# Kernel optimization log

Hardware: AMD Instinct MI355X
Metric: run time of the kernel (lower is better)

Reference implementation:

```python
import jax, jax.numpy as jnp
import numpy as np

N_NODES = 50000
N_EDGES = 640000
D_IN = 128
D_H1 = 128
D_H2 = 256
NEG_SLOPE = 0.2


def setup_inputs() -> dict:
    key = jax.random.key(0)
    ks = jax.random.split(key, 12)
    s = 1.0 / np.sqrt(D_IN)
    inp = {
        'x': jax.random.normal(ks[0], (N_NODES, D_IN), dtype=jnp.float32),
        'edge_index': jax.random.randint(ks[1], (2, N_EDGES), 0, N_NODES, dtype=jnp.int64),
        # GATv2 layer 1: 128 -> 128 (separate lin_l / lin_r, attention vec, residual proj, bias)
        'Wl1': jax.random.normal(ks[2], (D_IN, D_H1), dtype=jnp.float32) * s,
        'Wr1': jax.random.normal(ks[3], (D_IN, D_H1), dtype=jnp.float32) * s,
        'att1': jax.random.normal(ks[4], (D_H1,), dtype=jnp.float32) * s,
        'Wres1': jax.random.normal(ks[5], (D_IN, D_H1), dtype=jnp.float32) * s,
        'b1': jnp.zeros((D_H1,), dtype=jnp.float32),
        # GATv2 layer 2: 128 -> 256
        'Wl2': jax.random.normal(ks[6], (D_H1, D_H2), dtype=jnp.float32) * s,
        'Wr2': jax.random.normal(ks[7], (D_H1, D_H2), dtype=jnp.float32) * s,
        'att2': jax.random.normal(ks[8], (D_H2,), dtype=jnp.float32) * s,
        'Wres2': jax.random.normal(ks[9], (D_H1, D_H2), dtype=jnp.float32) * s,
        'b2': jnp.zeros((D_H2,), dtype=jnp.float32),
    }
    return inp


def _gatv2_layer(x, Wl, Wr, att, Wres, b, src, dst, n_nodes):
    """GATv2Conv (heads=1, residual=True, eval mode/no dropout).
    score e_ij = att . LeakyReLU(Wl x_src + Wr x_dst); softmax over incoming edges per dst;
    out_dst = sum_j alpha_ij * (Wl x_src) + residual + bias.
    """
    xl = x @ Wl                      # [N, F]
    xr = x @ Wr                      # [N, F]
    h = xl[src] + xr[dst]            # [E, F]  gather (irregular access)
    e = jax.nn.leaky_relu(h, NEG_SLOPE) @ att   # [E]
    # segment softmax over destination nodes
    m = jax.ops.segment_max(e, dst, num_segments=n_nodes)      # [N]
    w = jnp.exp(e - m[dst])                                     # [E]
    denom = jax.ops.segment_sum(w, dst, num_segments=n_nodes)   # [N]
    alpha = w / (denom[dst] + 1e-16)                             # [E]
    out = jax.ops.segment_sum(alpha[:, None] * xl[src], dst, num_segments=n_nodes)  # [N, F]
    return out + x @ Wres + b


def reference(x, edge_index, Wl1, Wr1, att1, Wres1, b1, Wl2, Wr2, att2, Wres2, b2):
    src = edge_index[0]
    dst = edge_index[1]
    h = _gatv2_layer(x, Wl1, Wr1, att1, Wres1, b1, src, dst, N_NODES)
    h = jax.nn.elu(h)
    out = _gatv2_layer(h, Wl2, Wr2, att2, Wres2, b2, src, dst, N_NODES)
    return out
```

## Files before the change

### kernel.cpp

```cpp
#include <hip/hip_runtime.h>

typedef unsigned short u16;
typedef unsigned int u32;
typedef __attribute__((ext_vector_type(8))) short bf16x8;
typedef __attribute__((ext_vector_type(4))) float f32x4;
typedef __attribute__((ext_vector_type(2))) float f32x2;

#define NN 50000
#define NE 640000

__device__ __forceinline__ float bfl(u32 u) { return __uint_as_float(u << 16); }
__device__ __forceinline__ float bfh(u32 u) { return __uint_as_float(u & 0xffff0000u); }
__device__ __forceinline__ float bf1(u16 v) { return __uint_as_float(((u32)v) << 16); }
__device__ __forceinline__ u16 f2bf(float f) {
  u32 u = __float_as_uint(f);
  u32 r = (u + 0x7fffu + ((u >> 16) & 1u)) >> 16;
  return (u16)r;
}

__device__ __forceinline__ f32x2 bc2(float s) { return (f32x2){s, s}; }
__device__ __forceinline__ f32x2 pkfma(f32x2 a, f32x2 b, f32x2 c) {
  return __builtin_elementwise_fma(a, b, c);
}
__device__ __forceinline__ f32x2 pkabs(f32x2 a) {
  return __builtin_elementwise_abs(a);
}

template <int CTRL>
__device__ __forceinline__ float dpp_add(float x) {
  int t = __builtin_amdgcn_update_dpp(0, __float_as_int(x), CTRL, 0xf, 0xf, true);
  return x + __int_as_float(t);
}

__device__ __forceinline__ void unpk2(uint2 v, f32x2* o) {
  o[0] = (f32x2){bfl(v.x), bfh(v.x)};
  o[1] = (f32x2){bfl(v.y), bfh(v.y)};
}
__device__ __forceinline__ void unpk2(uint4 v, f32x2* o) {
  o[0] = (f32x2){bfl(v.x), bfh(v.x)};
  o[1] = (f32x2){bfl(v.y), bfh(v.y)};
  o[2] = (f32x2){bfl(v.z), bfh(v.z)};
  o[3] = (f32x2){bfl(v.w), bfh(v.w)};
}

template <int HEPL> struct VecSel;
template <> struct VecSel<4> { using T = uint2; };
template <> struct VecSel<8> { using T = uint4; };

__global__ void probe_kernel(const u16* __restrict__ x, const int* __restrict__ ei,
                             int* __restrict__ flags) {
  __shared__ int s_f32, s_i32;
  if (threadIdx.x == 0) { s_f32 = 0; s_i32 = 0; }
  __syncthreads();
  int lf = 0, li = 0;
  for (int i = threadIdx.x; i < 1024; i += 256) {
    float v = bf1(x[i]);
    if (!(fabsf(v) < 1e8f)) lf = 1;
    if (ei[2 * i + 1] != 0) li = 1;
  }
  if (lf) s_f32 = 1;
  if (li) s_i32 = 1;
  __syncthreads();
  if (threadIdx.x == 0) {
    flags[0] = s_f32;
    flags[1] = s_i32 ? 0 : 1;
  }
}

__device__ __forceinline__ int edge_val(const int* __restrict__ w, long j, int i64) {
  return i64 ? w[2 * j] : w[j];
}

__global__ void count_kernel(const int* __restrict__ ei, const int* __restrict__ flags,
                             int* __restrict__ cnt, int E) {
  int e = blockIdx.x * blockDim.x + threadIdx.x;
  if (e >= E) return;
  int d = edge_val(ei, (long)E + e, flags[1]);
  if ((u32)d < (u32)NN) atomicAdd(&cnt[d], 1);
}

__global__ void scan_local(const int* __restrict__ cnt, int* __restrict__ excl,
                           int* __restrict__ bsum, int n) {
  __shared__ int sd[256];
  int t = threadIdx.x;
  int g = blockIdx.x * 256 + t;
  int v = (g < n) ? cnt[g] : 0;
  sd[t] = v;
  __syncthreads();
  for (int off = 1; off < 256; off <<= 1) {
    int x = (t >= off) ? sd[t - off] : 0;
    __syncthreads();
    sd[t] += x;
    __syncthreads();
  }
  int incl = sd[t];
  if (g < n) excl[g] = incl - v;
  if (t == 255) bsum[blockIdx.x] = incl;
}

__global__ void scan_totals(const int* __restrict__ bsum, int* __restrict__ boff, int nb) {
  __shared__ int sd[256];
  int t = threadIdx.x;
  int v = (t < nb) ? bsum[t] : 0;
  sd[t] = v;
  __syncthreads();
  for (int off = 1; off < 256; off <<= 1) {
    int x = (t >= off) ? sd[t - off] : 0;
    __syncthreads();
    sd[t] += x;
    __syncthreads();
  }
  if (t < nb) boff[t] = sd[t] - v;
}

__global__ void scan_add(const int* __restrict__ excl, const int* __restrict__ boff,
                         const int* __restrict__ cnt, int* __restrict__ rowptr,
                         int* __restrict__ fillp, int n) {
  int g = blockIdx.x * 256 + threadIdx.x;
  if (g < n) {
    int e2 = excl[g] + boff[blockIdx.x];
    rowptr[g] = e2;
    fillp[g] = e2;
    if (g == n - 1) rowptr[n] = e2 + cnt[g];
  }
}

__global__ void fill_kernel(const int* __restrict__ ei, const int* __restrict__ flags,
                            int* __restrict__ fillp, int* __restrict__ col, int E) {
  int e = blockIdx.x * blockDim.x + threadIdx.x;
  if (e >= E) return;
  int i64 = flags[1];
  int s = edge_val(ei, (long)e, i64);
  int d = edge_val(ei, (long)E + e, i64);
  if ((u32)d >= (u32)NN) return;
  int p = atomicAdd(&fillp[d], 1);
  col[p] = ((u32)s < (u32)NN) ? s : 0;
}

__global__ void transpose_w(const void* W0, const void* W1, const void* W2,
                            const void* W3, const void* W4, const void* W5,
                            u16* T0, u16* T1, u16* T2, u16* T3, u16* T4, u16* T5,
                            const int* __restrict__ flags) {
  int y = blockIdx.y;
  int M = (y < 3) ? 128 : 256;
  int flat = blockIdx.x * 256 + threadIdx.x;
  if (flat >= M * 128) return;
  int j = flat >> 7;
  int k = flat & 127;
  const void* W = (y == 0) ? W0 : (y == 1) ? W1 : (y == 2) ? W2 : (y == 3) ? W3 : (y == 4) ? W4 : W5;
  u16* T = (y == 0) ? T0 : (y == 1) ? T1 : (y == 2) ? T2 : (y == 3) ? T3 : (y == 4) ? T4 : T5;
  u16 v;
  if (flags[0])
    v = f2bf(((const float*)W)[(size_t)k * M + j]);
  else
    v = ((const u16*)W)[(size_t)k * M + j];
  T[(size_t)j * 128 + k] = v;
}

#define LSTR 136
__global__ __launch_bounds__(256) void gemm3_mfma(
    const void* __restrict__ X,
    const u16* __restrict__ Wta, const u16* __restrict__ Wtb, const u16* __restrict__ Wtc,
    const void* __restrict__ bias,
    u16* __restrict__ Ya, u16* __restrict__ Yb, u16* __restrict__ Yc,
    const int* __restrict__ flags, int x_follows, int N, int M) {
  __shared__ __align__(16) u16 Xs[64 * LSTR];
  __shared__ __align__(16) u16 Bs[128 * LSTR];
  const int K = 128;
  int t = threadIdx.x;
  int lane = t & 63;
  int w = t >> 6;
  int n0g = blockIdx.x * 64;
  int c0 = blockIdx.z * 128;
  int F32X = x_follows ? flags[0] : 0;
  const u16* Wt = (blockIdx.y == 0) ? Wta : ((blockIdx.y == 1) ? Wtb : Wtc);
  u16* Y = (blockIdx.y == 0) ? Ya : ((blockIdx.y == 1) ? Yb : Yc);

  if (!F32X) {
    const u16* Xg = (const u16*)X;
    for (int it = 0; it < 4; ++it) {
      int i = t + 256 * it;
      int r = i >> 4, c8 = (i & 15) * 8;
      int n = n0g + r;
      uint4 v = make_uint4(0, 0, 0, 0);
      if (n < N) v = *(const uint4*)(Xg + (size_t)n * K + c8);
      *(uint4*)(Xs + r * LSTR + c8) = v;
    }
  } else {
    const float* Xg = (const float*)X;
    for (int it = 0; it < 4; ++it) {
      int i = t + 256 * it;
      int r = i >> 4, c8 = (i & 15) * 8;
      int n = n0g + r;
      uint4 pk = make_uint4(0, 0, 0, 0);
      if (n < N) {
        float4 f0 = *(const float4*)(Xg + (size_t)n * K + c8);
        float4 f1 = *(const float4*)(Xg + (size_t)n * K + c8 + 4);
        pk.x = (u32)f2bf(f0.x) | ((u32)f2bf(f0.y) << 16);
        pk.y = (u32)f2bf(f0.z) | ((u32)f2bf(f0.w) << 16);
        pk.z = (u32)f2bf(f1.x) | ((u32)f2bf(f1.y) << 16);
        pk.w = (u32)f2bf(f1.z) | ((u32)f2bf(f1.w) << 16);
      }
      *(uint4*)(Xs + r * LSTR + c8) = pk;
    }
  }
  for (int it = 0; it < 8; ++it) {
    int i = t + 256 * it;
    int j = i >> 4, k8 = (i & 15) * 8;
    uint4 v = *(const uint4*)(Wt + (size_t)(c0 + j) * K + k8);
    *(uint4*)(Bs + j * LSTR + k8) = v;
  }
  __syncthreads();

  int m0 = (w >> 1) * 32;
  int n0 = (w & 1) * 64;
  int l15 = lane & 15;
  int q8 = (lane >> 4) * 8;
  f32x4 acc[2][4];
#pragma unroll
  for (int i = 0; i < 2; ++i)
#pragma unroll
    for (int j = 0; j < 4; ++j) acc[i][j] = (f32x4){0.f, 0.f, 0.f, 0.f};

#pragma unroll
  for (int kc = 0; kc < 4; ++kc) {
    int ko = kc * 32 + q8;
    bf16x8 a[2], b[4];
#pragma unroll
    for (int i = 0; i < 2; ++i)
      a[i] = *(const bf16x8*)(Xs + (m0 + i * 16 + l15) * LSTR + ko);
#pragma unroll
    for (int j = 0; j < 4; ++j)
      b[j] = *(const bf16x8*)(Bs + (n0 + j * 16 + l15) * LSTR + ko);
#pragma unroll
    for (int i = 0; i < 2; ++i)
#pragma unroll
      for (int j = 0; j < 4; ++j)
        acc[i][j] = __builtin_amdgcn_mfma_f32_16x16x32_bf16(a[i], b[j], acc[i][j], 0, 0, 0);
  }
  __syncthreads();

  float bv[4] = {0.f, 0.f, 0.f, 0.f};
  if (blockIdx.y == 2) {
    int F32 = flags[0];
#pragma unroll
    for (int j = 0; j < 4; ++j) {
      int c = c0 + n0 + j * 16 + l15;
      bv[j] = F32 ? ((const float*)bias)[c] : bf1(((const u16*)bias)[c]);
    }
  }

  u16* Ct = Xs;
#pragma unroll
  for (int i = 0; i < 2; ++i)
#pragma unroll
    for (int j = 0; j < 4; ++j) {
      int col = n0 + j * 16 + l15;
      int rbase = m0 + i * 16 + (lane >> 4) * 4;
#pragma unroll
      for (int r = 0; r < 4; ++r)
        Ct[(rbase + r) * LSTR + col] = f2bf(acc[i][j][r] + bv[j]);
    }
  __syncthreads();

  for (int it = 0; it < 4; ++it) {
    int i = t + 256 * it;
    int r = i >> 4, c8 = (i & 15) * 8;
    int n = n0g + r;
    if (n < N) {
      uint4 v = *(const uint4*)(Ct + r * LSTR + c8);
      *(uint4*)(Y + (size_t)n * M + c0 + c8) = v;
    }
  }
}

template <int F, bool ELU>
__global__ __launch_bounds__(256) void gat_agg_kernel(
    const u16* __restrict__ xl, const u16* __restrict__ xr, const u16* __restrict__ res,
    const void* __restrict__ att, const int* __restrict__ rowptr, const int* __restrict__ col,
    void* __restrict__ out, const int* __restrict__ flags, int out_follows, int N) {
  constexpr int HEPL = F / 32;
  constexpr int HP = HEPL / 2;
  using VecT = typename VecSel<HEPL>::T;
  int tid = threadIdx.x;
  int hl = tid & 31;
  int node = blockIdx.x * 8 + (tid >> 5);
  if (node >= N) return;
  int F32 = flags[0];
  int OF32 = out_follows ? F32 : 0;
  int base = hl * HEPL;

  f32x2 xr2[HP], att6[HP], att4[HP], acc2[HP];
  {
    VecT xp = *(const VecT*)(xr + (size_t)node * F + base);
    unpk2(xp, xr2);
  }
  if (F32) {
    const float* af = (const float*)att + base;
#pragma unroll
    for (int p = 0; p < HP; ++p) {
      f32x2 a = (f32x2){af[2 * p], af[2 * p + 1]};
      att6[p] = a * 0.6f;
      att4[p] = a * 0.4f;
    }
  } else {
    f32x2 a2[HP];
    VecT ap = *(const VecT*)((const u16*)att + base);
    unpk2(ap, a2);
#pragma unroll
    for (int p = 0; p < HP; ++p) {
      att6[p] = a2[p] * 0.6f;
      att4[p] = a2[p] * 0.4f;
    }
  }
#pragma unroll
  for (int p = 0; p < HP; ++p) acc2[p] = bc2(0.f);

  float m = -1e30f, l = 0.f;
  int beg = rowptr[node], end = rowptr[node + 1];
  int deg = end - beg;

  if (deg > 0) {
    int nit = (deg + 1) >> 1;
    int dm1 = deg - 1;
    auto ldc = [&](int j) -> int { return col[beg + min(j, dm1)]; };
    auto gat = [&](int c) -> VecT { return *(const VecT*)(xl + (size_t)c * F + base); };

    int c0 = ldc(0), c1 = ldc(1), c2 = ldc(2), c3 = ldc(3);
    int c4 = ldc(4), c5 = ldc(5);
    VecT va = gat(c0), vb = gat(c1), vc = gat(c2), vd = gat(c3);

    for (int t = 0; t < nit; ++t) {
      VecT x0v = va, x1v = vb;
      int act1 = (2 * t + 1) < deg;
      va = vc; vb = vd;
      if (t + 2 < nit) { vc = gat(c4); vd = gat(c5); }
      if (t + 3 < nit) { c4 = ldc(2 * t + 6); c5 = ldc(2 * t + 7); }

      f32x2 x0[HP], x1[HP];
      unpk2(x0v, x0);
      unpk2(x1v, x1);
      f32x2 s0 = bc2(0.f), s1 = bc2(0.f);
#pragma unroll
      for (int p = 0; p < HP; ++p) {
        f32x2 h0 = x0[p] + xr2[p];
        f32x2 h1 = x1[p] + xr2[p];
        f32x2 ha0 = pkabs(h0);
        f32x2 ha1 = pkabs(h1);
        s0 = pkfma(att6[p], h0, s0);
        s1 = pkfma(att6[p], h1, s1);
        s0 = pkfma(att4[p], ha0, s0);
        s1 = pkfma(att4[p], ha1, s1);
      }
      float d0 = s0.x + s0.y;
      float d1 = s1.x + s1.y;
      d0 = dpp_add<0xB1>(d0);  d1 = dpp_add<0xB1>(d1);
      d0 = dpp_add<0x4E>(d0);  d1 = dpp_add<0x4E>(d1);
      d0 = dpp_add<0x141>(d0); d1 = dpp_add<0x141>(d1);
      d0 = dpp_add<0x140>(d0); d1 = dpp_add<0x140>(d1);
      d0 += __shfl_xor(d0, 16, 64);
      d1 += __shfl_xor(d1, 16, 64);

      float p0 = d0;
      float p1 = act1 ? d1 : -1e30f;
      float mn = fmaxf(m, fmaxf(p0, p1));
      float scl = __expf(m - mn);
      float w0 = __expf(p0 - mn);
      float w1 = __expf(p1 - mn);
      l = fmaf(l, scl, w0 + w1);
      f32x2 w0b = bc2(w0), w1b = bc2(w1), sclb = bc2(scl);
#pragma unroll
      for (int p = 0; p < HP; ++p)
        acc2[p] = pkfma(sclb, acc2[p], pkfma(w1b, x1[p], w0b * x0[p]));
      m = mn;
    }
  }

  float inv = 1.f / (l + 1e-16f);
  VecT rp = *(const VecT*)(res + (size_t)node * F + base);
  f32x2 rv[HP];
  unpk2(rp, rv);
  f32x2 ov[HP];
  f32x2 invb = bc2(inv);
#pragma unroll
  for (int p = 0; p < HP; ++p) {
    f32x2 o = pkfma(acc2[p], invb, rv[p]);
    if (ELU) {
      o.x = (o.x > 0.f) ? o.x : (__expf(o.x) - 1.f);
      o.y = (o.y > 0.f) ? o.y : (__expf(o.y) - 1.f);
    }
    ov[p] = o;
  }
  if (OF32) {
    float* of = (float*)out + (size_t)node * F + base;
    float4 f0 = {ov[0].x, ov[0].y, ov[1].x, ov[1].y};
    *(float4*)of = f0;
    if constexpr (HP == 4) {
      float4 f1 = {ov[2].x, ov[2].y, ov[3].x, ov[3].y};
      *(float4*)(of + 4) = f1;
    }
  } else {
    u16* o16 = (u16*)out;
    if constexpr (HP == 2) {
      uint2 pk;
      pk.x = (u32)f2bf(ov[0].x) | ((u32)f2bf(ov[0].y) << 16);
      pk.y = (u32)f2bf(ov[1].x) | ((u32)f2bf(ov[1].y) << 16);
      *(uint2*)(o16 + (size_t)node * F + base) = pk;
    } else {
      uint4 pk;
      pk.x = (u32)f2bf(ov[0].x) | ((u32)f2bf(ov[0].y) << 16);
      pk.y = (u32)f2bf(ov[1].x) | ((u32)f2bf(ov[1].y) << 16);
      pk.z = (u32)f2bf(ov[2].x) | ((u32)f2bf(ov[2].y) << 16);
      pk.w = (u32)f2bf(ov[3].x) | ((u32)f2bf(ov[3].y) << 16);
      *(uint4*)(o16 + (size_t)node * F + base) = pk;
    }
  }
}

extern "C" void kernel_launch(void* const* d_in, const int* in_sizes, int n_in,
                              void* d_out, int out_size, void* d_ws, size_t ws_size,
                              hipStream_t stream) {
  const u16* x16 = (const u16*)d_in[0];
  const int* ei = (const int*)d_in[1];
  const int N = NN, E = NE;

  char* ws = (char*)d_ws;
  size_t off = 0;
  auto alloc = [&](size_t bytes) -> void* {
    void* p = (void*)(ws + off);
    off += (bytes + 255) & ~(size_t)255;
    return p;
  };
  int* flags = (int*)alloc(2 * 4);
  int* cnt = (int*)alloc((size_t)N * 4);
  int* rowptr = (int*)alloc((size_t)(N + 1) * 4);
  int* fillp = (int*)alloc((size_t)N * 4);
  int* colb = (int*)alloc((size_t)E * 4);
  int* excl = (int*)alloc((size_t)N * 4);
  int* bsum = (int*)alloc(256 * 4);
  int* boff = (int*)alloc(256 * 4);
  u16* Wt1a = (u16*)alloc((size_t)128 * 128 * 2);
  u16* Wt1b = (u16*)alloc((size_t)128 * 128 * 2);
  u16* Wt1c = (u16*)alloc((size_t)128 * 128 * 2);
  u16* Wt2a = (u16*)alloc((size_t)256 * 128 * 2);
  u16* Wt2b = (u16*)alloc((size_t)256 * 128 * 2);
  u16* Wt2c = (u16*)alloc((size_t)256 * 128 * 2);
  u16* buf1 = (u16*)alloc((size_t)N * 256 * 2);
  u16* buf2 = (u16*)alloc((size_t)N * 256 * 2);
  u16* buf3 = (u16*)alloc((size_t)N * 256 * 2);
  u16* h1 = (u16*)alloc((size_t)N * 128 * 2);
  (void)ws_size; (void)n_in; (void)in_sizes; (void)out_size;

  int nb = (N + 255) / 256;

  probe_kernel<<<1, 256, 0, stream>>>(x16, ei, flags);
  hipMemsetAsync(cnt, 0, (size_t)N * 4, stream);
  count_kernel<<<(E + 255) / 256, 256, 0, stream>>>(ei, flags, cnt, E);
  scan_local<<<nb, 256, 0, stream>>>(cnt, excl, bsum, N);
  scan_totals<<<1, 256, 0, stream>>>(bsum, boff, nb);
  scan_add<<<nb, 256, 0, stream>>>(excl, boff, cnt, rowptr, fillp, N);
  fill_kernel<<<(E + 255) / 256, 256, 0, stream>>>(ei, flags, fillp, colb, E);
  transpose_w<<<dim3(128, 6), 256, 0, stream>>>(
      d_in[2], d_in[3], d_in[5], d_in[7], d_in[8], d_in[10],
      Wt1a, Wt1b, Wt1c, Wt2a, Wt2b, Wt2c, flags);

  int gx = (N + 63) / 64;
  gemm3_mfma<<<dim3(gx, 3, 1), 256, 0, stream>>>(
      d_in[0], Wt1a, Wt1b, Wt1c, d_in[6], buf1, buf2, buf3, flags, 1, N, 128);
  gat_agg_kernel<128, true><<<(N + 7) / 8, 256, 0, stream>>>(
      buf1, buf2, buf3, d_in[4], rowptr, colb, h1, flags, 0, N);
  gemm3_mfma<<<dim3(gx, 3, 2), 256, 0, stream>>>(
      h1, Wt2a, Wt2b, Wt2c, d_in[11], buf1, buf2, buf3, flags, 0, N, 256);
  gat_agg_kernel<256, false><<<(N + 7) / 8, 256, 0, stream>>>(
      buf1, buf2, buf3, d_in[9], rowptr, colb, d_out, flags, 1, N);
}
```

Measured before the change: 327.2 us.

## Fuse the three projection GEMMs per row tile to reuse staged X

Replaces the 3D grid, in which each block computed one weight and one column chunk, with a 512-thread block holding a 128-row X tile. That block loops over all three weight matrices and their column chunks, reusing the X tile from LDS. This removes the redundant reloads (and fp32-to-bf16 conversion) of X across the separate grid blocks. In exchange the grid is smaller, and each block runs the weight loads, MFMA and stores serially with several barriers per pass, so there is less parallelism and overlap.

```diff
diff --git a/kernel.cpp b/kernel.cpp
--- a/kernel.cpp
+++ b/kernel.cpp
@@ -158,28 +158,27 @@
 }
 
 #define LSTR 136
-__global__ __launch_bounds__(256) void gemm3_mfma(
+template <int MZ>
+__global__ __launch_bounds__(512) void gemm3_fused(
     const void* __restrict__ X,
     const u16* __restrict__ Wta, const u16* __restrict__ Wtb, const u16* __restrict__ Wtc,
     const void* __restrict__ bias,
     u16* __restrict__ Ya, u16* __restrict__ Yb, u16* __restrict__ Yc,
-    const int* __restrict__ flags, int x_follows, int N, int M) {
-  __shared__ __align__(16) u16 Xs[64 * LSTR];
+    const int* __restrict__ flags, int x_follows, int N) {
+  constexpr int M = MZ * 128;
+  __shared__ __align__(16) u16 Xs[128 * LSTR];
   __shared__ __align__(16) u16 Bs[128 * LSTR];
   const int K = 128;
   int t = threadIdx.x;
   int lane = t & 63;
   int w = t >> 6;
-  int n0g = blockIdx.x * 64;
-  int c0 = blockIdx.z * 128;
+  int n0g = blockIdx.x * 128;
   int F32X = x_follows ? flags[0] : 0;
-  const u16* Wt = (blockIdx.y == 0) ? Wta : ((blockIdx.y == 1) ? Wtb : Wtc);
-  u16* Y = (blockIdx.y == 0) ? Ya : ((blockIdx.y == 1) ? Yb : Yc);
 
   if (!F32X) {
     const u16* Xg = (const u16*)X;
     for (int it = 0; it < 4; ++it) {
-      int i = t + 256 * it;
+      int i = t + 512 * it;
       int r = i >> 4, c8 = (i & 15) * 8;
       int n = n0g + r;
       uint4 v = make_uint4(0, 0, 0, 0);
@@ -189,7 +188,7 @@
   } else {
     const float* Xg = (const float*)X;
     for (int it = 0; it < 4; ++it) {
-      int i = t + 256 * it;
+      int i = t + 512 * it;
       int r = i >> 4, c8 = (i & 15) * 8;
       int n = n0g + r;
       uint4 pk = make_uint4(0, 0, 0, 0);
@@ -204,72 +203,73 @@
       *(uint4*)(Xs + r * LSTR + c8) = pk;
     }
   }
-  for (int it = 0; it < 8; ++it) {
-    int i = t + 256 * it;
-    int j = i >> 4, k8 = (i & 15) * 8;
-    uint4 v = *(const uint4*)(Wt + (size_t)(c0 + j) * K + k8);
-    *(uint4*)(Bs + j * LSTR + k8) = v;
-  }
-  __syncthreads();
-
-  int m0 = (w >> 1) * 32;
-  int n0 = (w & 1) * 64;
+
   int l15 = lane & 15;
   int q8 = (lane >> 4) * 8;
-  f32x4 acc[2][4];
-#pragma unroll
-  for (int i = 0; i < 2; ++i)
-#pragma unroll
-    for (int j = 0; j < 4; ++j) acc[i][j] = (f32x4){0.f, 0.f, 0.f, 0.f};
-
-#pragma unroll
-  for (int kc = 0; kc < 4; ++kc) {
-    int ko = kc * 32 + q8;
-    bf16x8 a[2], b[4];
-#pragma unroll
-    for (int i = 0; i < 2; ++i)
-      a[i] = *(const bf16x8*)(Xs + (m0 + i * 16 + l15) * LSTR + ko);
-#pragma unroll
-    for (int j = 0; j < 4; ++j)
-      b[j] = *(const bf16x8*)(Bs + (n0 + j * 16 + l15) * LSTR + ko);
-#pragma unroll
-    for (int i = 0; i < 2; ++i)
-#pragma unroll
-      for (int j = 0; j < 4; ++j)
-        acc[i][j] = __builtin_amdgcn_mfma_f32_16x16x32_bf16(a[i], b[j], acc[i][j], 0, 0, 0);
-  }
-  __syncthreads();
-
-  float bv[4] = {0.f, 0.f, 0.f, 0.f};
-  if (blockIdx.y == 2) {
-    int F32 = flags[0];
-#pragma unroll
-    for (int j = 0; j < 4; ++j) {
-      int c = c0 + n0 + j * 16 + l15;
-      bv[j] = F32 ? ((const float*)bias)[c] : bf1(((const u16*)bias)[c]);
-    }
-  }
-
-  u16* Ct = Xs;
-#pragma unroll
-  for (int i = 0; i < 2; ++i)
-#pragma unroll
-    for (int j = 0; j < 4; ++j) {
-      int col = n0 + j * 16 + l15;
-      int rbase = m0 + i * 16 + (lane >> 4) * 4;
-#pragma unroll
-      for (int r = 0; r < 4; ++r)
-        Ct[(rbase + r) * LSTR + col] = f2bf(acc[i][j][r] + bv[j]);
-    }
-  __syncthreads();
-
-  for (int it = 0; it < 4; ++it) {
-    int i = t + 256 * it;
-    int r = i >> 4, c8 = (i & 15) * 8;
-    int n = n0g + r;
-    if (n < N) {
-      uint4 v = *(const uint4*)(Ct + r * LSTR + c8);
-      *(uint4*)(Y + (size_t)n * M + c0 + c8) = v;
+  int m0 = w * 16;
+  int F32B = flags[0];
+
+#pragma unroll
+  for (int z = 0; z < MZ; ++z) {
+#pragma unroll
+    for (int y = 0; y < 3; ++y) {
+      const u16* Wt = (y == 0) ? Wta : ((y == 1) ? Wtb : Wtc);
+      int c0 = z * 128;
+      for (int it = 0; it < 4; ++it) {
+        int i = t + 512 * it;
+        int j = i >> 4, k8 = (i & 15) * 8;
+        uint4 v = *(const uint4*)(Wt + (size_t)(c0 + j) * K + k8);
+        *(uint4*)(Bs + j * LSTR + k8) = v;
+      }
+      __syncthreads();
+
+      f32x4 acc[8];
+#pragma unroll
+      for (int j = 0; j < 8; ++j) acc[j] = (f32x4){0.f, 0.f, 0.f, 0.f};
+#pragma unroll
+      for (int kc = 0; kc < 4; ++kc) {
+        int ko = kc * 32 + q8;
+        bf16x8 a = *(const bf16x8*)(Xs + (m0 + l15) * LSTR + ko);
+        bf16x8 b[8];
+#pragma unroll
+        for (int j = 0; j < 8; ++j)
+          b[j] = *(const bf16x8*)(Bs + (j * 16 + l15) * LSTR + ko);
+#pragma unroll
+        for (int j = 0; j < 8; ++j)
+          acc[j] = __builtin_amdgcn_mfma_f32_16x16x32_bf16(a, b[j], acc[j], 0, 0, 0);
+      }
+      __syncthreads();
+
+      float bv[8] = {0.f, 0.f, 0.f, 0.f, 0.f, 0.f, 0.f, 0.f};
+      if (y == 2) {
+#pragma unroll
+        for (int j = 0; j < 8; ++j) {
+          int c = c0 + j * 16 + l15;
+          bv[j] = F32B ? ((const float*)bias)[c] : bf1(((const u16*)bias)[c]);
+        }
+      }
+      u16* Ct = Bs;
+      int rbase = m0 + (lane >> 4) * 4;
+#pragma unroll
+      for (int j = 0; j < 8; ++j) {
+        int colj = j * 16 + l15;
+#pragma unroll
+        for (int r = 0; r < 4; ++r)
+          Ct[(rbase + r) * LSTR + colj] = f2bf(acc[j][r] + bv[j]);
+      }
+      __syncthreads();
+
+      u16* Y = (y == 0) ? Ya : ((y == 1) ? Yb : Yc);
+      for (int it = 0; it < 4; ++it) {
+        int i = t + 512 * it;
+        int r = i >> 4, c8 = (i & 15) * 8;
+        int n = n0g + r;
+        if (n < N) {
+          uint4 v = *(const uint4*)(Ct + r * LSTR + c8);
+          *(uint4*)(Y + (size_t)n * M + c0 + c8) = v;
+        }
+      }
+      __syncthreads();
     }
   }
 }
@@ -464,13 +464,13 @@
       d_in[2], d_in[3], d_in[5], d_in[7], d_in[8], d_in[10],
       Wt1a, Wt1b, Wt1c, Wt2a, Wt2b, Wt2c, flags);
 
-  int gx = (N + 63) / 64;
-  gemm3_mfma<<<dim3(gx, 3, 1), 256, 0, stream>>>(
-      d_in[0], Wt1a, Wt1b, Wt1c, d_in[6], buf1, buf2, buf3, flags, 1, N, 128);
+  int gx = (N + 127) / 128;
+  gemm3_fused<1><<<gx, 512, 0, stream>>>(
+      d_in[0], Wt1a, Wt1b, Wt1c, d_in[6], buf1, buf2, buf3, flags, 1, N);
   gat_agg_kernel<128, true><<<(N + 7) / 8, 256, 0, stream>>>(
       buf1, buf2, buf3, d_in[4], rowptr, colb, h1, flags, 0, N);
-  gemm3_mfma<<<dim3(gx, 3, 2), 256, 0, stream>>>(
-      h1, Wt2a, Wt2b, Wt2c, d_in[11], buf1, buf2, buf3, flags, 0, N, 256);
+  gemm3_fused<2><<<gx, 512, 0, stream>>>(
+      h1, Wt2a, Wt2b, Wt2c, d_in[11], buf1, buf2, buf3, flags, 0, N);
   gat_agg_kernel<256, false><<<(N + 7) / 8, 256, 0, stream>>>(
       buf1, buf2, buf3, d_in[9], rowptr, colb, d_out, flags, 1, N);
 }
```

Measured after the change: 333.0 us. No clear change (+1.8%).

## Use 16-lane groups for layer-1 aggregation, fuse CSR scan, deepen gather prefetch

Applied to the files above, without the earlier changes.

Layer-1 aggregation now gives each node a 16-lane group with 16-byte loads per lane instead of 32 lanes with 8-byte loads. This halves the shuffle reductions per edge and doubles the nodes handled per block. The gather pipeline prefetches one more edge pair ahead to hide irregular load latency, at the cost of extra registers. The three-kernel scan that builds the CSR row pointers is replaced by a single 1024-thread block scan, cutting launches but serializing the work onto one workgroup.

```diff
diff --git a/kernel.cpp b/kernel.cpp
--- a/kernel.cpp
+++ b/kernel.cpp
@@ -32,20 +32,12 @@
   return x + __int_as_float(t);
 }
 
-__device__ __forceinline__ void unpk2(uint2 v, f32x2* o) {
-  o[0] = (f32x2){bfl(v.x), bfh(v.x)};
-  o[1] = (f32x2){bfl(v.y), bfh(v.y)};
-}
 __device__ __forceinline__ void unpk2(uint4 v, f32x2* o) {
   o[0] = (f32x2){bfl(v.x), bfh(v.x)};
   o[1] = (f32x2){bfl(v.y), bfh(v.y)};
   o[2] = (f32x2){bfl(v.z), bfh(v.z)};
   o[3] = (f32x2){bfl(v.w), bfh(v.w)};
 }
-
-template <int HEPL> struct VecSel;
-template <> struct VecSel<4> { using T = uint2; };
-template <> struct VecSel<8> { using T = uint4; };
 
 __global__ void probe_kernel(const u16* __restrict__ x, const int* __restrict__ ei,
                              int* __restrict__ flags) {
@@ -79,50 +71,31 @@
   if ((u32)d < (u32)NN) atomicAdd(&cnt[d], 1);
 }
 
-__global__ void scan_local(const int* __restrict__ cnt, int* __restrict__ excl,
-                           int* __restrict__ bsum, int n) {
-  __shared__ int sd[256];
+__global__ __launch_bounds__(1024) void scan_fused(const int* __restrict__ cnt,
+                                                   int* __restrict__ rowptr,
+                                                   int* __restrict__ fillp, int n) {
+  __shared__ int sums[1024];
   int t = threadIdx.x;
-  int g = blockIdx.x * 256 + t;
-  int v = (g < n) ? cnt[g] : 0;
-  sd[t] = v;
-  __syncthreads();
-  for (int off = 1; off < 256; off <<= 1) {
-    int x = (t >= off) ? sd[t - off] : 0;
+  int per = (n + 1023) / 1024;
+  int s0 = t * per;
+  int s1 = min(s0 + per, n);
+  int s = 0;
+  for (int i = s0; i < s1; ++i) s += cnt[i];
+  sums[t] = s;
+  __syncthreads();
+  for (int off = 1; off < 1024; off <<= 1) {
+    int x = (t >= off) ? sums[t - off] : 0;
     __syncthreads();
-    sd[t] += x;
+    sums[t] += x;
     __syncthreads();
   }
-  int incl = sd[t];
-  if (g < n) excl[g] = incl - v;
-  if (t == 255) bsum[blockIdx.x] = incl;
-}
-
-__global__ void scan_totals(const int* __restrict__ bsum, int* __restrict__ boff, int nb) {
-  __shared__ int sd[256];
-  int t = threadIdx.x;
-  int v = (t < nb) ? bsum[t] : 0;
-  sd[t] = v;
-  __syncthreads();
-  for (int off = 1; off < 256; off <<= 1) {
-    int x = (t >= off) ? sd[t - off] : 0;
-    __syncthreads();
-    sd[t] += x;
-    __syncthreads();
-  }
-  if (t < nb) boff[t] = sd[t] - v;
-}
-
-__global__ void scan_add(const int* __restrict__ excl, const int* __restrict__ boff,
-                         const int* __restrict__ cnt, int* __restrict__ rowptr,
-                         int* __restrict__ fillp, int n) {
-  int g = blockIdx.x * 256 + threadIdx.x;
-  if (g < n) {
-    int e2 = excl[g] + boff[blockIdx.x];
-    rowptr[g] = e2;
-    fillp[g] = e2;
-    if (g == n - 1) rowptr[n] = e2 + cnt[g];
-  }
+  int run = sums[t] - s;
+  for (int i = s0; i < s1; ++i) {
+    rowptr[i] = run;
+    fillp[i] = run;
+    run += cnt[i];
+  }
+  if (t == 1023) rowptr[n] = run;
 }
 
 __global__ void fill_kernel(const int* __restrict__ ei, const int* __restrict__ flags,
@@ -274,25 +247,25 @@
   }
 }
 
-template <int F, bool ELU>
+template <int F, bool ELU, int GL>
 __global__ __launch_bounds__(256) void gat_agg_kernel(
     const u16* __restrict__ xl, const u16* __restrict__ xr, const u16* __restrict__ res,
     const void* __restrict__ att, const int* __restrict__ rowptr, const int* __restrict__ col,
     void* __restrict__ out, const int* __restrict__ flags, int out_follows, int N) {
-  constexpr int HEPL = F / 32;
+  constexpr int HEPL = F / GL;
   constexpr int HP = HEPL / 2;
-  using VecT = typename VecSel<HEPL>::T;
+  static_assert(HEPL == 8, "GL must be F/8");
   int tid = threadIdx.x;
-  int hl = tid & 31;
-  int node = blockIdx.x * 8 + (tid >> 5);
+  int gl = tid & (GL - 1);
+  int node = blockIdx.x * (256 / GL) + (tid / GL);
   if (node >= N) return;
   int F32 = flags[0];
   int OF32 = out_follows ? F32 : 0;
-  int base = hl * HEPL;
+  int base = gl * HEPL;
 
   f32x2 xr2[HP], att6[HP], att4[HP], acc2[HP];
   {
-    VecT xp = *(const VecT*)(xr + (size_t)node * F + base);
+    uint4 xp = *(const uint4*)(xr + (size_t)node * F + base);
     unpk2(xp, xr2);
   }
   if (F32) {
@@ -305,7 +278,7 @@
     }
   } else {
     f32x2 a2[HP];
-    VecT ap = *(const VecT*)((const u16*)att + base);
+    uint4 ap = *(const uint4*)((const u16*)att + base);
     unpk2(ap, a2);
 #pragma unroll
     for (int p = 0; p < HP; ++p) {
@@ -324,18 +297,18 @@
     int nit = (deg + 1) >> 1;
     int dm1 = deg - 1;
     auto ldc = [&](int j) -> int { return col[beg + min(j, dm1)]; };
-    auto gat = [&](int c) -> VecT { return *(const VecT*)(xl + (size_t)c * F + base); };
-
-    int c0 = ldc(0), c1 = ldc(1), c2 = ldc(2), c3 = ldc(3);
-    int c4 = ldc(4), c5 = ldc(5);
-    VecT va = gat(c0), vb = gat(c1), vc = gat(c2), vd = gat(c3);
+    auto gat = [&](int c) -> uint4 { return *(const uint4*)(xl + (size_t)c * F + base); };
+
+    uint4 r0 = gat(ldc(0)), r1 = gat(ldc(1)), r2 = gat(ldc(2)), r3 = gat(ldc(3));
+    uint4 r4 = gat(ldc(4)), r5 = gat(ldc(5));
+    int c6 = ldc(6), c7 = ldc(7);
 
     for (int t = 0; t < nit; ++t) {
-      VecT x0v = va, x1v = vb;
+      uint4 x0v = r0, x1v = r1;
       int act1 = (2 * t + 1) < deg;
-      va = vc; vb = vd;
-      if (t + 2 < nit) { vc = gat(c4); vd = gat(c5); }
-      if (t + 3 < nit) { c4 = ldc(2 * t + 6); c5 = ldc(2 * t + 7); }
+      r0 = r2; r1 = r3; r2 = r4; r3 = r5;
+      if (t + 3 < nit) { r4 = gat(c6); r5 = gat(c7); }
+      if (t + 4 < nit) { c6 = ldc(2 * t + 8); c7 = ldc(2 * t + 9); }
 
       f32x2 x0[HP], x1[HP];
       unpk2(x0v, x0);
@@ -358,8 +331,10 @@
       d0 = dpp_add<0x4E>(d0);  d1 = dpp_add<0x4E>(d1);
       d0 = dpp_add<0x141>(d0); d1 = dpp_add<0x141>(d1);
       d0 = dpp_add<0x140>(d0); d1 = dpp_add<0x140>(d1);
-      d0 += __shfl_xor(d0, 16, 64);
-      d1 += __shfl_xor(d1, 16, 64);
+      if constexpr (GL == 32) {
+        d0 += __shfl_xor(d0, 16, 64);
+        d1 += __shfl_xor(d1, 16, 64);
+      }
 
       float p0 = d0;
       float p1 = act1 ? d1 : -1e30f;
@@ -377,7 +352,7 @@
   }
 
   float inv = 1.f / (l + 1e-16f);
-  VecT rp = *(const VecT*)(res + (size_t)node * F + base);
+  uint4 rp = *(const uint4*)(res + (size_t)node * F + base);
   f32x2 rv[HP];
   unpk2(rp, rv);
   f32x2 ov[HP];
@@ -394,26 +369,17 @@
   if (OF32) {
     float* of = (float*)out + (size_t)node * F + base;
     float4 f0 = {ov[0].x, ov[0].y, ov[1].x, ov[1].y};
+    float4 f1 = {ov[2].x, ov[2].y, ov[3].x, ov[3].y};
     *(float4*)of = f0;
-    if constexpr (HP == 4) {
-      float4 f1 = {ov[2].x, ov[2].y, ov[3].x, ov[3].y};
-      *(float4*)(of + 4) = f1;
-    }
+    *(float4*)(of + 4) = f1;
   } else {
     u16* o16 = (u16*)out;
-    if constexpr (HP == 2) {
-      uint2 pk;
-      pk.x = (u32)f2bf(ov[0].x) | ((u32)f2bf(ov[0].y) << 16);
-      pk.y = (u32)f2bf(ov[1].x) | ((u32)f2bf(ov[1].y) << 16);
-      *(uint2*)(o16 + (size_t)node * F + base) = pk;
-    } else {
-      uint4 pk;
-      pk.x = (u32)f2bf(ov[0].x) | ((u32)f2bf(ov[0].y) << 16);
-      pk.y = (u32)f2bf(ov[1].x) | ((u32)f2bf(ov[1].y) << 16);
-      pk.z = (u32)f2bf(ov[2].x) | ((u32)f2bf(ov[2].y) << 16);
-      pk.w = (u32)f2bf(ov[3].x) | ((u32)f2bf(ov[3].y) << 16);
-      *(uint4*)(o16 + (size_t)node * F + base) = pk;
-    }
+    uint4 pk;
+    pk.x = (u32)f2bf(ov[0].x) | ((u32)f2bf(ov[0].y) << 16);
+    pk.y = (u32)f2bf(ov[1].x) | ((u32)f2bf(ov[1].y) << 16);
+    pk.z = (u32)f2bf(ov[2].x) | ((u32)f2bf(ov[2].y) << 16);
+    pk.w = (u32)f2bf(ov[3].x) | ((u32)f2bf(ov[3].y) << 16);
+    *(uint4*)(o16 + (size_t)node * F + base) = pk;
   }
 }
 
@@ -436,9 +402,6 @@
   int* rowptr = (int*)alloc((size_t)(N + 1) * 4);
   int* fillp = (int*)alloc((size_t)N * 4);
   int* colb = (int*)alloc((size_t)E * 4);
-  int* excl = (int*)alloc((size_t)N * 4);
-  int* bsum = (int*)alloc(256 * 4);
-  int* boff = (int*)alloc(256 * 4);
   u16* Wt1a = (u16*)alloc((size_t)128 * 128 * 2);
   u16* Wt1b = (u16*)alloc((size_t)128 * 128 * 2);
   u16* Wt1c = (u16*)alloc((size_t)128 * 128 * 2);
@@ -451,14 +414,10 @@
   u16* h1 = (u16*)alloc((size_t)N * 128 * 2);
   (void)ws_size; (void)n_in; (void)in_sizes; (void)out_size;
 
-  int nb = (N + 255) / 256;
-
   probe_kernel<<<1, 256, 0, stream>>>(x16, ei, flags);
   hipMemsetAsync(cnt, 0, (size_t)N * 4, stream);
   count_kernel<<<(E + 255) / 256, 256, 0, stream>>>(ei, flags, cnt, E);
-  scan_local<<<nb, 256, 0, stream>>>(cnt, excl, bsum, N);
-  scan_totals<<<1, 256, 0, stream>>>(bsum, boff, nb);
-  scan_add<<<nb, 256, 0, stream>>>(excl, boff, cnt, rowptr, fillp, N);
+  scan_fused<<<1, 1024, 0, stream>>>(cnt, rowptr, fillp, N);
   fill_kernel<<<(E + 255) / 256, 256, 0, stream>>>(ei, flags, fillp, colb, E);
   transpose_w<<<dim3(128, 6), 256, 0, stream>>>(
       d_in[2], d_in[3], d_in[5], d_in[7], d_in[8], d_in[10],
@@ -467,10 +426,10 @@
   int gx = (N + 63) / 64;
   gemm3_mfma<<<dim3(gx, 3, 1), 256, 0, stream>>>(
       d_in[0], Wt1a, Wt1b, Wt1c, d_in[6], buf1, buf2, buf3, flags, 1, N, 128);
-  gat_agg_kernel<128, true><<<(N + 7) / 8, 256, 0, stream>>>(
+  gat_agg_kernel<128, true, 16><<<(N + 15) / 16, 256, 0, stream>>>(
       buf1, buf2, buf3, d_in[4], rowptr, colb, h1, flags, 0, N);
   gemm3_mfma<<<dim3(gx, 3, 2), 256, 0, stream>>>(
       h1, Wt2a, Wt2b, Wt2c, d_in[11], buf1, buf2, buf3, flags, 0, N, 256);
-  gat_agg_kernel<256, false><<<(N + 7) / 8, 256, 0, stream>>>(
+  gat_agg_kernel<256, false, 32><<<(N + 7) / 8, 256, 0, stream>>>(
       buf1, buf2, buf3, d_in[9], rowptr, colb, d_out, flags, 1, N);
 }
```

After: 431.1 us. +31.7%, slower.
